# Kernel optimization log

Hardware: AMD Instinct MI355X
Metric: run time of the kernel (lower is better)

## Reference

```python
import jax, jax.numpy as jnp
import numpy as np

N = 200000          # occupied pillars
H = W = 512         # pseudo_image_dims
C = 32              # feat_channels == embed_dim
HEADS = 2
DH = C // HEADS     # 16
SHIFTS = np.array([[0, 0], [-1, 0], [1, 0], [0, 1], [-1, 1], [1, 1], [0, -1], [-1, -1], [1, -1]], dtype=np.int32)  # INDEX_SHIFT, 9 neighbors


def setup_inputs() -> dict:
    key = jax.random.key(0)
    ks = jax.random.split(key, 7)
    # unique BEV cells so the coord->index lookup is well defined
    perm = jax.random.permutation(ks[0], H * W)[:N]
    bev_coors = jnp.stack([perm // W, perm % W], axis=1).astype(jnp.int32)  # [N,2] (row, col)
    return {
        "voxel_feats": jax.random.normal(ks[1], (N, C), dtype=jnp.float32),
        "bev_coors": bev_coors,
        "pos_embedding": jax.random.normal(ks[2], (9, C), dtype=jnp.float32) * 0.02,
        "w_qkv": jax.random.normal(ks[3], (3 * C, C), dtype=jnp.float32) * 0.05,
        "b_qkv": jax.random.normal(ks[4], (3 * C,), dtype=jnp.float32) * 0.01,
        "w_out": jax.random.normal(ks[5], (C, C), dtype=jnp.float32) * 0.05,
        "b_out": jax.random.normal(ks[6], (C,), dtype=jnp.float32) * 0.01,
    }


def reference(voxel_feats, bev_coors, pos_embedding, w_qkv, b_qkv, w_out, b_out):
    shifts = jnp.asarray(SHIFTS)
    # dense lookup grid: (row, col) -> voxel index, -1 if empty
    grid = jnp.full((H, W), -1, dtype=jnp.int32)
    grid = grid.at[bev_coors[:, 0], bev_coors[:, 1]].set(jnp.arange(N, dtype=jnp.int32))

    # 9-neighbor gather with out-of-grid / empty-cell masking
    shifted = bev_coors[:, None, :] + shifts[None, :, :]                     # [N,9,2]
    in_bounds = ((shifted[..., 0] >= 0) & (shifted[..., 0] < H) &
                 (shifted[..., 1] >= 0) & (shifted[..., 1] < W))             # [N,9]
    sc = jnp.clip(shifted, 0, jnp.array([H - 1, W - 1], dtype=jnp.int32))
    nbr_idx = grid[sc[..., 0], sc[..., 1]]                                    # [N,9]
    nbr_idx = jnp.where(in_bounds, nbr_idx, -1)
    # gather neighbor feats, add per-shift positional embedding, zero invalid (masked_fill)
    kv = voxel_feats[jnp.clip(nbr_idx, 0, N - 1)] + pos_embedding[None, :, :]  # [N,9,C]
    kv = jnp.where((nbr_idx >= 0)[..., None], kv, 0.0)

    # multi-head attention: query = own feat (len 1), key/value = 9 neighbors
    wq, wk, wv = w_qkv[:C], w_qkv[C:2 * C], w_qkv[2 * C:]
    bq, bk, bv = b_qkv[:C], b_qkv[C:2 * C], b_qkv[2 * C:]
    q = (voxel_feats @ wq.T + bq).reshape(N, HEADS, DH)                      # [N,h,d]
    k = (kv @ wk.T + bk).reshape(N, 9, HEADS, DH)                            # [N,9,h,d]
    v = (kv @ wv.T + bv).reshape(N, 9, HEADS, DH)
    scores = jnp.einsum('nhd,nkhd->nhk', q, k) / jnp.sqrt(jnp.float32(DH))   # [N,h,9]
    attn = jax.nn.softmax(scores, axis=-1)
    out = jnp.einsum('nhk,nkhd->nhd', attn, v).reshape(N, C)
    out = out @ w_out.T + b_out                                              # [N,C]

    # concat and scatter to BEV pseudo-image [1, 2C, H, W]
    feat = jnp.concatenate([voxel_feats, out], axis=1)                       # [N,2C]
    canvas = jnp.zeros((2 * C, H, W), dtype=feat.dtype)
    canvas = canvas.at[:, bev_coors[:, 0], bev_coors[:, 1]].set(feat.T)
    return canvas[None]
```

## Files before the change

kernel.cpp:

```cpp
#include <hip/hip_runtime.h>
#include <hip/hip_bf16.h>

#define H_ 512
#define W_ 512
#define C_ 32
#define NPOS_ (H_ * W_)
#define TX_ 32
#define TY_ 8
#define HXX_ 34
#define HYY_ 10
#define NCELL_ (HXX_ * HYY_)
#define FST_ 40

#define CW_M 0
#define CW_U 2048
#define CW_P 2112
#define CW_R 4160

typedef float v2f __attribute__((ext_vector_type(2)));
typedef float f32x4_t __attribute__((ext_vector_type(4)));
typedef short bf16x8 __attribute__((ext_vector_type(8)));

static __device__ __forceinline__ v2f pk_add(v2f a, v2f b) {
    v2f d; asm("v_pk_add_f32 %0, %1, %2" : "=v"(d) : "v"(a), "v"(b)); return d;
}
static __device__ __forceinline__ v2f pk_fma(v2f a, v2f b, v2f c) {
    v2f d; asm("v_pk_fma_f32 %0, %1, %2, %3" : "=v"(d) : "v"(a), "v"(b), "v"(c)); return d;
}
static __device__ __forceinline__ unsigned cvt_pk_bf16(float lo, float hi) {
    unsigned r; asm("v_cvt_pk_bf16_f32 %0, %1, %2" : "=v"(r) : "v"(lo), "v"(hi)); return r;
}
static __device__ __forceinline__ short f2bf(float v) {
    __hip_bfloat16 h = __float2bfloat16(v);
    return *reinterpret_cast<short*>(&h);
}
static __device__ __forceinline__ int q_sidx(int pos, int c) {
    return pos * 64 + ((((c >> 3) ^ (pos & 7))) << 3) + (c & 7);
}
#define WFENCE() do { asm volatile("s_waitcnt lgkmcnt(0)" ::: "memory"); \
                      __builtin_amdgcn_sched_barrier(0); } while (0)

__global__ __launch_bounds__(256) void build_grid_k(const int* __restrict__ coors,
                                                    int* __restrict__ grid, int n) {
    int i = blockIdx.x * 256 + threadIdx.x;
    if (i < n) {
        int y = coors[2 * i + 0];
        int x = coors[2 * i + 1];
        grid[y * W_ + x] = i;
    }
}

__global__ __launch_bounds__(256) void prep_k(int4* __restrict__ grid4,
                                              const float* __restrict__ wqkv,
                                              const float* __restrict__ bqkv,
                                              const float* __restrict__ wout,
                                              const float* __restrict__ bout,
                                              float* __restrict__ cw) {
    if (blockIdx.x < 256) {
        grid4[blockIdx.x * 256 + threadIdx.x] = int4{-1, -1, -1, -1};
        return;
    }
    const int e0 = (int)(blockIdx.x - 256) * 256 + threadIdx.x;
    if (e0 < 2048) {
        const int i = e0 >> 6, c = e0 & 63;
        const int h = c >> 5, j = c & 31;
        float s = 0.f;
        for (int d = 0; d < 16; ++d)
            s += wqkv[(h * 16 + d) * 32 + i] * wqkv[(32 + h * 16 + d) * 32 + j];
        cw[CW_M + e0] = s;
    } else if (e0 < 4096) {
        const int e = e0 - 2048;
        const int srow = e >> 5, c = e & 31;
        const int h = srow >> 5, j = srow & 31;
        float s = 0.f;
        for (int d = 0; d < 16; ++d)
            s += wout[c * 32 + h * 16 + d] * wqkv[(64 + h * 16 + d) * 32 + j];
        cw[CW_P + e] = s;
    } else if (e0 < 4160) {
        const int e = e0 - 4096;
        const int h = e >> 5, j = e & 31;
        float s = 0.f;
        for (int d = 0; d < 16; ++d)
            s += bqkv[h * 16 + d] * wqkv[(32 + h * 16 + d) * 32 + j];
        cw[CW_U + e] = s;
    } else if (e0 < 4192) {
        const int c = e0 - 4160;
        float s = bout[c];
        for (int dv = 0; dv < 32; ++dv)
            s += wout[c * 32 + dv] * bqkv[64 + dv];
        cw[CW_R + c] = s;
    }
}

__global__ __launch_bounds__(256, 2) void fused_k(const float* __restrict__ feats,
                                                  const int* __restrict__ grid,
                                                  const float* __restrict__ pe,
                                                  const float* __restrict__ cw,
                                                  float* __restrict__ canvas) {
    __shared__ __align__(16) short flds[NCELL_ * FST_];
    __shared__ __align__(16) short qlds[256 * 64];
    __shared__ int vlds[NCELL_];
    __shared__ float pelds[288];

    const int tid = threadIdx.x;
    const int bid = blockIdx.x;
    const int tx0 = (bid & 15) * TX_;
    const int ty0 = (bid >> 4) * TY_;
    const int l15 = tid & 15;
    const int g4 = (tid >> 4) & 3;
    const int wv = tid >> 6;

    bf16x8 Bm[4];
#pragma unroll
    for (int ct = 0; ct < 4; ++ct) {
        bf16x8 b;
#pragma unroll
        for (int e = 0; e < 8; ++e)
            b[e] = f2bf(cw[CW_M + (8 * g4 + e) * 64 + ct * 16 + l15]);
        Bm[ct] = b;
    }
    bf16x8 Bp[2][2];
#pragma unroll
    for (int kc = 0; kc < 2; ++kc)
#pragma unroll
        for (int ct = 0; ct < 2; ++ct) {
            bf16x8 b;
#pragma unroll
            for (int e = 0; e < 8; ++e)
                b[e] = f2bf(cw[CW_P + (kc * 32 + 8 * g4 + e) * 32 + ct * 16 + l15]);
            Bp[kc][ct] = b;
        }
    float uq[4];
#pragma unroll
    for (int ct = 0; ct < 4; ++ct) uq[ct] = cw[CW_U + ct * 16 + l15];
    float rch[2];
#pragma unroll
    for (int ct = 0; ct < 2; ++ct) rch[ct] = cw[CW_R + ct * 16 + l15];

    for (int c = tid; c < 288; c += 256) pelds[c] = pe[c];
    for (int c = tid; c < NCELL_; c += 256) {
        const int hy = c / HXX_, hx = c - hy * HXX_;
        const int gy = ty0 + hy - 1, gx = tx0 + hx - 1;
        int vi = -1;
        if (((unsigned)gy < (unsigned)H_) && ((unsigned)gx < (unsigned)W_))
            vi = grid[gy * W_ + gx];
        vlds[c] = vi;
        uint4 wq[4];
        if (vi >= 0) {
            const float* src = feats + (size_t)vi * 32;
#pragma unroll
            for (int q = 0; q < 4; ++q) {
                const float4 va = *reinterpret_cast<const float4*>(src + q * 8);
                const float4 vb = *reinterpret_cast<const float4*>(src + q * 8 + 4);
                wq[q].x = cvt_pk_bf16(va.x, va.y);
                wq[q].y = cvt_pk_bf16(va.z, va.w);
                wq[q].z = cvt_pk_bf16(vb.x, vb.y);
                wq[q].w = cvt_pk_bf16(vb.z, vb.w);
            }
        } else {
            wq[0] = wq[1] = wq[2] = wq[3] = uint4{0u, 0u, 0u, 0u};
        }
#pragma unroll
        for (int q = 0; q < 4; ++q)
            *reinterpret_cast<uint4*>(flds + c * FST_ + q * 8) = wq[q];
    }
    __syncthreads();

    f32x4_t accq[4][4];
#pragma unroll
    for (int i = 0; i < 4; ++i) {
        const int rt = wv * 4 + i;
        const int pr = rt * 16 + l15;
        const int oc = ((pr >> 5) + 1) * HXX_ + (pr & 31) + 1;
        const bf16x8 af = *reinterpret_cast<const bf16x8*>(flds + oc * FST_ + 8 * g4);
#pragma unroll
        for (int ct = 0; ct < 4; ++ct) {
            f32x4_t acc = {uq[ct], uq[ct], uq[ct], uq[ct]};
            accq[i][ct] = __builtin_amdgcn_mfma_f32_16x16x32_bf16(af, Bm[ct], acc, 0, 0, 0);
        }
    }
#pragma unroll
    for (int i = 0; i < 4; ++i) {
        const int p0 = (wv * 4 + i) * 16 + g4 * 4;
#pragma unroll
        for (int ct = 0; ct < 4; ++ct) {
            const int c = ct * 16 + l15;
            const unsigned w01 = cvt_pk_bf16(accq[i][ct][0], accq[i][ct][1]);
            const unsigned w23 = cvt_pk_bf16(accq[i][ct][2], accq[i][ct][3]);
            qlds[q_sidx(p0 + 0, c)] = (short)(w01 & 0xffffu);
            qlds[q_sidx(p0 + 1, c)] = (short)(w01 >> 16);
            qlds[q_sidx(p0 + 2, c)] = (short)(w23 & 0xffffu);
            qlds[q_sidx(p0 + 3, c)] = (short)(w23 >> 16);
        }
    }
    WFENCE();

    const int lx = tid & 31, ly = tid >> 5;
    const int p = (ty0 + ly) * W_ + tx0 + lx;
    const int pos = tid;
    const int ocell = (ly + 1) * HXX_ + lx + 1;
    const bool occ = vlds[ocell] >= 0;

    {
        const short* fb = flds + ocell * FST_;
#pragma unroll
        for (int q = 0; q < 4; ++q) {
            const uint4 w = *reinterpret_cast<const uint4*>(fb + q * 8);
            const unsigned uu[4] = {w.x, w.y, w.z, w.w};
#pragma unroll
            for (int d = 0; d < 4; ++d) {
                const int j = q * 8 + d * 2;
                canvas[(size_t)j * NPOS_ + p] = __uint_as_float(uu[d] << 16);
                canvas[(size_t)(j + 1) * NPOS_ + p] = __uint_as_float(uu[d] & 0xffff0000u);
            }
        }
    }

    if (occ) {
        v2f qk0[16], qk1[16];
#pragma unroll
        for (int cb = 0; cb < 8; ++cb) {
            const uint4 w = *reinterpret_cast<const uint4*>(qlds + pos * 64 + ((cb ^ (pos & 7)) << 3));
            const unsigned uu[4] = {w.x, w.y, w.z, w.w};
#pragma unroll
            for (int d = 0; d < 4; ++d) {
                const int jj = cb * 4 + d;
                v2f qv;
                qv.x = __uint_as_float(uu[d] << 16);
                qv.y = __uint_as_float(uu[d] & 0xffff0000u);
                if (jj < 16) qk0[jj] = qv; else qk1[jj - 16] = qv;
            }
        }
        float l0 = 0.f, l1 = 0.f;
        v2f g0[16], g1[16];
#pragma unroll
        for (int j = 0; j < 16; ++j) { g0[j] = v2f{0.f, 0.f}; g1[j] = v2f{0.f, 0.f}; }

        const int DYv[9] = {0, -1, 1, 0, -1, 1, 0, -1, 1};
        const int DXv[9] = {0, 0, 0, 1, 1, 1, -1, -1, -1};
#pragma unroll
        for (int k = 0; k < 9; ++k) {
            const int cell = (ly + 1 + DYv[k]) * HXX_ + (lx + 1 + DXv[k]);
            const bool val = vlds[cell] >= 0;
            const short* fb = flds + cell * FST_;
            v2f t[16];
#pragma unroll
            for (int q = 0; q < 4; ++q) {
                const uint4 w = *reinterpret_cast<const uint4*>(fb + q * 8);
                const unsigned uu[4] = {w.x, w.y, w.z, w.w};
#pragma unroll
                for (int d = 0; d < 4; ++d) {
                    const int jj = q * 4 + d;
                    v2f tv;
                    tv.x = __uint_as_float(uu[d] << 16);
                    tv.y = __uint_as_float(uu[d] & 0xffff0000u);
                    t[jj] = pk_add(tv, *reinterpret_cast<const v2f*>(pelds + k * 32 + 2 * jj));
                }
            }
            v2f sp0{0.f, 0.f}, sp1{0.f, 0.f};
#pragma unroll
            for (int j = 0; j < 16; ++j) {
                sp0 = pk_fma(qk0[j], t[j], sp0);
                sp1 = pk_fma(qk1[j], t[j], sp1);
            }
            const float e0 = __expf((sp0.x + sp0.y) * 0.25f);
            const float e1 = __expf((sp1.x + sp1.y) * 0.25f);
            l0 += val ? e0 : 1.f;
            l1 += val ? e1 : 1.f;
            const float w0 = val ? e0 : 0.f;
            const float w1 = val ? e1 : 0.f;
            const v2f w0v{w0, w0}, w1v{w1, w1};
#pragma unroll
            for (int j = 0; j < 16; ++j) {
                g0[j] = pk_fma(w0v, t[j], g0[j]);
                g1[j] = pk_fma(w1v, t[j], g1[j]);
            }
        }
        const float inv0 = 1.f / l0, inv1 = 1.f / l1;
#pragma unroll
        for (int cb = 0; cb < 8; ++cb) {
            unsigned wd[4];
#pragma unroll
            for (int d = 0; d < 4; ++d) {
                const int jj = cb * 4 + d;
                const v2f gg = (jj < 16) ? g0[jj] : g1[jj - 16];
                const float iv = (jj < 16) ? inv0 : inv1;
                wd[d] = cvt_pk_bf16(gg.x * iv, gg.y * iv);
            }
            const uint4 w{wd[0], wd[1], wd[2], wd[3]};
            *reinterpret_cast<uint4*>(qlds + pos * 64 + ((cb ^ (pos & 7)) << 3)) = w;
        }
    } else {
        const uint4 z{0u, 0u, 0u, 0u};
#pragma unroll
        for (int cb = 0; cb < 8; ++cb)
            *reinterpret_cast<uint4*>(qlds + pos * 64 + ((cb ^ (pos & 7)) << 3)) = z;
    }
    WFENCE();

    f32x4_t acco[4][2];
#pragma unroll
    for (int i = 0; i < 4; ++i) {
        const int pr = (wv * 4 + i) * 16 + l15;
        const bf16x8 a0 = *reinterpret_cast<const bf16x8*>(qlds + pr * 64 + (((0 + g4) ^ (pr & 7)) << 3));
        const bf16x8 a1 = *reinterpret_cast<const bf16x8*>(qlds + pr * 64 + (((4 + g4) ^ (pr & 7)) << 3));
#pragma unroll
        for (int ct = 0; ct < 2; ++ct) {
            f32x4_t acc = {0.f, 0.f, 0.f, 0.f};
            acc = __builtin_amdgcn_mfma_f32_16x16x32_bf16(a0, Bp[0][ct], acc, 0, 0, 0);
            acc = __builtin_amdgcn_mfma_f32_16x16x32_bf16(a1, Bp[1][ct], acc, 0, 0, 0);
            acco[i][ct] = acc;
        }
    }
#pragma unroll
    for (int i = 0; i < 4; ++i) {
        const int pt0 = (wv * 4 + i) * 16 + g4 * 4;
        const int yy = pt0 >> 5, xx = pt0 & 31;
        bool ok[4];
#pragma unroll
        for (int r = 0; r < 4; ++r) {
            const int pt = pt0 + r;
            ok[r] = vlds[((pt >> 5) + 1) * HXX_ + (pt & 31) + 1] >= 0;
        }
#pragma unroll
        for (int ct = 0; ct < 2; ++ct) {
            const int ch = 32 + ct * 16 + l15;
            float4 ov;
            ov.x = ok[0] ? acco[i][ct][0] + rch[ct] : 0.f;
            ov.y = ok[1] ? acco[i][ct][1] + rch[ct] : 0.f;
            ov.z = ok[2] ? acco[i][ct][2] + rch[ct] : 0.f;
            ov.w = ok[3] ? acco[i][ct][3] + rch[ct] : 0.f;
            *reinterpret_cast<float4*>(&canvas[(size_t)ch * NPOS_ + (ty0 + yy) * W_ + tx0 + xx]) = ov;
        }
    }
}

extern "C" void kernel_launch(void* const* d_in, const int* in_sizes, int n_in,
                              void* d_out, int out_size, void* d_ws, size_t ws_size,
                              hipStream_t stream) {
    const float* feats = (const float*)d_in[0];
    const int*   coors = (const int*)d_in[1];
    const float* pe    = (const float*)d_in[2];
    const float* wqkv  = (const float*)d_in[3];
    const float* bqkv  = (const float*)d_in[4];
    const float* wout  = (const float*)d_in[5];
    const float* bout  = (const float*)d_in[6];
    float* canvas = (float*)d_out;

    const int n = in_sizes[0] / C_;
    int* grid = (int*)d_ws;
    float* cw = (float*)((char*)d_ws + NPOS_ * sizeof(int));

    prep_k<<<273, 256, 0, stream>>>((int4*)grid, wqkv, bqkv, wout, bout, cw);
    build_grid_k<<<(n + 255) / 256, 256, 0, stream>>>(coors, grid, n);
    fused_k<<<(W_ / TX_) * (H_ / TY_), 256, 0, stream>>>(feats, grid, pe, cw, canvas);
}
```

Baseline: 46.80 us.

## Split attention into two passes with per-head threads to halve LDS and registers

Restructures the fused kernel so each wave handles its 64 positions in two batches of 32. The query projection, the attention and the output projection run per batch. Within a batch each thread computes one head for one position instead of both heads, which halves per-thread register arrays. The q buffer in LDS shrinks to 128 rows, and launch bounds are raised to 3 blocks per CU to gain occupancy. In exchange there are more wave fences and loop iterations, each neighbor feature is loaded and unpacked twice (once per head), and the extra occupancy may force register spills.

After: 74.97 us. 60.2% more time.

```diff
diff --git a/kernel.cpp b/kernel.cpp
--- a/kernel.cpp
+++ b/kernel.cpp
@@ -34,8 +34,8 @@
     __hip_bfloat16 h = __float2bfloat16(v);
     return *reinterpret_cast<short*>(&h);
 }
-static __device__ __forceinline__ int q_sidx(int pos, int c) {
-    return pos * 64 + ((((c >> 3) ^ (pos & 7))) << 3) + (c & 7);
+static __device__ __forceinline__ int q_sidx(int row, int c) {
+    return row * 64 + ((((c >> 3) ^ (row & 7))) << 3) + (c & 7);
 }
 #define WFENCE() do { asm volatile("s_waitcnt lgkmcnt(0)" ::: "memory"); \
                       __builtin_amdgcn_sched_barrier(0); } while (0)
@@ -92,13 +92,13 @@
     }
 }
 
-__global__ __launch_bounds__(256, 2) void fused_k(const float* __restrict__ feats,
+__global__ __launch_bounds__(256, 3) void fused_k(const float* __restrict__ feats,
                                                   const int* __restrict__ grid,
                                                   const float* __restrict__ pe,
                                                   const float* __restrict__ cw,
                                                   float* __restrict__ canvas) {
     __shared__ __align__(16) short flds[NCELL_ * FST_];
-    __shared__ __align__(16) short qlds[256 * 64];
+    __shared__ __align__(16) short qlds[128 * 64];
     __shared__ int vlds[NCELL_];
     __shared__ float pelds[288];
 
@@ -166,43 +166,10 @@
     }
     __syncthreads();
 
-    f32x4_t accq[4][4];
-#pragma unroll
-    for (int i = 0; i < 4; ++i) {
-        const int rt = wv * 4 + i;
-        const int pr = rt * 16 + l15;
-        const int oc = ((pr >> 5) + 1) * HXX_ + (pr & 31) + 1;
-        const bf16x8 af = *reinterpret_cast<const bf16x8*>(flds + oc * FST_ + 8 * g4);
-#pragma unroll
-        for (int ct = 0; ct < 4; ++ct) {
-            f32x4_t acc = {uq[ct], uq[ct], uq[ct], uq[ct]};
-            accq[i][ct] = __builtin_amdgcn_mfma_f32_16x16x32_bf16(af, Bm[ct], acc, 0, 0, 0);
-        }
-    }
-#pragma unroll
-    for (int i = 0; i < 4; ++i) {
-        const int p0 = (wv * 4 + i) * 16 + g4 * 4;
-#pragma unroll
-        for (int ct = 0; ct < 4; ++ct) {
-            const int c = ct * 16 + l15;
-            const unsigned w01 = cvt_pk_bf16(accq[i][ct][0], accq[i][ct][1]);
-            const unsigned w23 = cvt_pk_bf16(accq[i][ct][2], accq[i][ct][3]);
-            qlds[q_sidx(p0 + 0, c)] = (short)(w01 & 0xffffu);
-            qlds[q_sidx(p0 + 1, c)] = (short)(w01 >> 16);
-            qlds[q_sidx(p0 + 2, c)] = (short)(w23 & 0xffffu);
-            qlds[q_sidx(p0 + 3, c)] = (short)(w23 >> 16);
-        }
-    }
-    WFENCE();
-
-    const int lx = tid & 31, ly = tid >> 5;
-    const int p = (ty0 + ly) * W_ + tx0 + lx;
-    const int pos = tid;
-    const int ocell = (ly + 1) * HXX_ + lx + 1;
-    const bool occ = vlds[ocell] >= 0;
-
     {
-        const short* fb = flds + ocell * FST_;
+        const int lx = tid & 31, ly = tid >> 5;
+        const int p = (ty0 + ly) * W_ + tx0 + lx;
+        const short* fb = flds + ((ly + 1) * HXX_ + lx + 1) * FST_;
 #pragma unroll
         for (int q = 0; q < 4; ++q) {
             const uint4 w = *reinterpret_cast<const uint4*>(fb + q * 8);
@@ -216,122 +183,151 @@
         }
     }
 
-    if (occ) {
-        v2f qk0[16], qk1[16];
-#pragma unroll
-        for (int cb = 0; cb < 8; ++cb) {
-            const uint4 w = *reinterpret_cast<const uint4*>(qlds + pos * 64 + ((cb ^ (pos & 7)) << 3));
-            const unsigned uu[4] = {w.x, w.y, w.z, w.w};
-#pragma unroll
-            for (int d = 0; d < 4; ++d) {
-                const int jj = cb * 4 + d;
-                v2f qv;
-                qv.x = __uint_as_float(uu[d] << 16);
-                qv.y = __uint_as_float(uu[d] & 0xffff0000u);
-                if (jj < 16) qk0[jj] = qv; else qk1[jj - 16] = qv;
-            }
-        }
-        float l0 = 0.f, l1 = 0.f;
-        v2f g0[16], g1[16];
-#pragma unroll
-        for (int j = 0; j < 16; ++j) { g0[j] = v2f{0.f, 0.f}; g1[j] = v2f{0.f, 0.f}; }
-
-        const int DYv[9] = {0, -1, 1, 0, -1, 1, 0, -1, 1};
-        const int DXv[9] = {0, 0, 0, 1, 1, 1, -1, -1, -1};
-#pragma unroll
-        for (int k = 0; k < 9; ++k) {
-            const int cell = (ly + 1 + DYv[k]) * HXX_ + (lx + 1 + DXv[k]);
-            const bool val = vlds[cell] >= 0;
-            const short* fb = flds + cell * FST_;
-            v2f t[16];
-#pragma unroll
-            for (int q = 0; q < 4; ++q) {
-                const uint4 w = *reinterpret_cast<const uint4*>(fb + q * 8);
-                const unsigned uu[4] = {w.x, w.y, w.z, w.w};
-#pragma unroll
-                for (int d = 0; d < 4; ++d) {
-                    const int jj = q * 4 + d;
-                    v2f tv;
-                    tv.x = __uint_as_float(uu[d] << 16);
-                    tv.y = __uint_as_float(uu[d] & 0xffff0000u);
-                    t[jj] = pk_add(tv, *reinterpret_cast<const v2f*>(pelds + k * 32 + 2 * jj));
+    const int DYv[9] = {0, -1, 1, 0, -1, 1, 0, -1, 1};
+    const int DXv[9] = {0, 0, 0, 1, 1, 1, -1, -1, -1};
+    const int hh = (tid >> 5) & 1;
+    const int m31 = tid & 31;
+    const int qrow0 = wv * 32;
+
+    for (int b = 0; b < 2; ++b) {
+#pragma unroll
+        for (int ii = 0; ii < 2; ++ii) {
+            const int pr = (wv * 4 + b * 2 + ii) * 16 + l15;
+            const int oc = ((pr >> 5) + 1) * HXX_ + (pr & 31) + 1;
+            const bf16x8 af = *reinterpret_cast<const bf16x8*>(flds + oc * FST_ + 8 * g4);
+            f32x4_t accq[4];
+#pragma unroll
+            for (int ct = 0; ct < 4; ++ct) {
+                f32x4_t acc = {uq[ct], uq[ct], uq[ct], uq[ct]};
+                accq[ct] = __builtin_amdgcn_mfma_f32_16x16x32_bf16(af, Bm[ct], acc, 0, 0, 0);
+            }
+            const int r0 = qrow0 + ii * 16 + g4 * 4;
+#pragma unroll
+            for (int ct = 0; ct < 4; ++ct) {
+                const int c = ct * 16 + l15;
+                const unsigned w01 = cvt_pk_bf16(accq[ct][0], accq[ct][1]);
+                const unsigned w23 = cvt_pk_bf16(accq[ct][2], accq[ct][3]);
+                qlds[q_sidx(r0 + 0, c)] = (short)(w01 & 0xffffu);
+                qlds[q_sidx(r0 + 1, c)] = (short)(w01 >> 16);
+                qlds[q_sidx(r0 + 2, c)] = (short)(w23 & 0xffffu);
+                qlds[q_sidx(r0 + 3, c)] = (short)(w23 >> 16);
+            }
+        }
+        WFENCE();
+
+        {
+            const int pos = wv * 64 + b * 32 + m31;
+            const int ply = pos >> 5, plx = pos & 31;
+            const int socell = (ply + 1) * HXX_ + plx + 1;
+            const int srow = qrow0 + m31;
+            if (vlds[socell] >= 0) {
+                v2f qk[16];
+#pragma unroll
+                for (int cc = 0; cc < 4; ++cc) {
+                    const uint4 w = *reinterpret_cast<const uint4*>(
+                        qlds + srow * 64 + (((4 * hh + cc) ^ (srow & 7)) << 3));
+                    const unsigned uu[4] = {w.x, w.y, w.z, w.w};
+#pragma unroll
+                    for (int d = 0; d < 4; ++d) {
+                        v2f qv;
+                        qv.x = __uint_as_float(uu[d] << 16);
+                        qv.y = __uint_as_float(uu[d] & 0xffff0000u);
+                        qk[cc * 4 + d] = qv;
+                    }
                 }
-            }
-            v2f sp0{0.f, 0.f}, sp1{0.f, 0.f};
-#pragma unroll
-            for (int j = 0; j < 16; ++j) {
-                sp0 = pk_fma(qk0[j], t[j], sp0);
-                sp1 = pk_fma(qk1[j], t[j], sp1);
-            }
-            const float e0 = __expf((sp0.x + sp0.y) * 0.25f);
-            const float e1 = __expf((sp1.x + sp1.y) * 0.25f);
-            l0 += val ? e0 : 1.f;
-            l1 += val ? e1 : 1.f;
-            const float w0 = val ? e0 : 0.f;
-            const float w1 = val ? e1 : 0.f;
-            const v2f w0v{w0, w0}, w1v{w1, w1};
-#pragma unroll
-            for (int j = 0; j < 16; ++j) {
-                g0[j] = pk_fma(w0v, t[j], g0[j]);
-                g1[j] = pk_fma(w1v, t[j], g1[j]);
-            }
-        }
-        const float inv0 = 1.f / l0, inv1 = 1.f / l1;
-#pragma unroll
-        for (int cb = 0; cb < 8; ++cb) {
-            unsigned wd[4];
-#pragma unroll
-            for (int d = 0; d < 4; ++d) {
-                const int jj = cb * 4 + d;
-                const v2f gg = (jj < 16) ? g0[jj] : g1[jj - 16];
-                const float iv = (jj < 16) ? inv0 : inv1;
-                wd[d] = cvt_pk_bf16(gg.x * iv, gg.y * iv);
-            }
-            const uint4 w{wd[0], wd[1], wd[2], wd[3]};
-            *reinterpret_cast<uint4*>(qlds + pos * 64 + ((cb ^ (pos & 7)) << 3)) = w;
-        }
-    } else {
-        const uint4 z{0u, 0u, 0u, 0u};
-#pragma unroll
-        for (int cb = 0; cb < 8; ++cb)
-            *reinterpret_cast<uint4*>(qlds + pos * 64 + ((cb ^ (pos & 7)) << 3)) = z;
-    }
-    WFENCE();
-
-    f32x4_t acco[4][2];
-#pragma unroll
-    for (int i = 0; i < 4; ++i) {
-        const int pr = (wv * 4 + i) * 16 + l15;
-        const bf16x8 a0 = *reinterpret_cast<const bf16x8*>(qlds + pr * 64 + (((0 + g4) ^ (pr & 7)) << 3));
-        const bf16x8 a1 = *reinterpret_cast<const bf16x8*>(qlds + pr * 64 + (((4 + g4) ^ (pr & 7)) << 3));
-#pragma unroll
-        for (int ct = 0; ct < 2; ++ct) {
-            f32x4_t acc = {0.f, 0.f, 0.f, 0.f};
-            acc = __builtin_amdgcn_mfma_f32_16x16x32_bf16(a0, Bp[0][ct], acc, 0, 0, 0);
-            acc = __builtin_amdgcn_mfma_f32_16x16x32_bf16(a1, Bp[1][ct], acc, 0, 0, 0);
-            acco[i][ct] = acc;
-        }
-    }
-#pragma unroll
-    for (int i = 0; i < 4; ++i) {
-        const int pt0 = (wv * 4 + i) * 16 + g4 * 4;
-        const int yy = pt0 >> 5, xx = pt0 & 31;
-        bool ok[4];
-#pragma unroll
-        for (int r = 0; r < 4; ++r) {
-            const int pt = pt0 + r;
-            ok[r] = vlds[((pt >> 5) + 1) * HXX_ + (pt & 31) + 1] >= 0;
-        }
-#pragma unroll
-        for (int ct = 0; ct < 2; ++ct) {
-            const int ch = 32 + ct * 16 + l15;
-            float4 ov;
-            ov.x = ok[0] ? acco[i][ct][0] + rch[ct] : 0.f;
-            ov.y = ok[1] ? acco[i][ct][1] + rch[ct] : 0.f;
-            ov.z = ok[2] ? acco[i][ct][2] + rch[ct] : 0.f;
-            ov.w = ok[3] ? acco[i][ct][3] + rch[ct] : 0.f;
-            *reinterpret_cast<float4*>(&canvas[(size_t)ch * NPOS_ + (ty0 + yy) * W_ + tx0 + xx]) = ov;
-        }
+                float l = 0.f;
+                v2f g[16];
+#pragma unroll
+                for (int m = 0; m < 16; ++m) g[m] = v2f{0.f, 0.f};
+
+#pragma unroll
+                for (int k = 0; k < 9; ++k) {
+                    const int cell = (ply + 1 + DYv[k]) * HXX_ + (plx + 1 + DXv[k]);
+                    const bool val = vlds[cell] >= 0;
+                    const short* fb = flds + cell * FST_;
+                    v2f t[16];
+#pragma unroll
+                    for (int q = 0; q < 4; ++q) {
+                        const uint4 w = *reinterpret_cast<const uint4*>(fb + q * 8);
+                        const unsigned uu[4] = {w.x, w.y, w.z, w.w};
+#pragma unroll
+                        for (int d = 0; d < 4; ++d) {
+                            const int jj = q * 4 + d;
+                            v2f tv;
+                            tv.x = __uint_as_float(uu[d] << 16);
+                            tv.y = __uint_as_float(uu[d] & 0xffff0000u);
+                            t[jj] = pk_add(tv, *reinterpret_cast<const v2f*>(
+                                pelds + k * 32 + 2 * jj));
+                        }
+                    }
+                    v2f sp{0.f, 0.f};
+#pragma unroll
+                    for (int m = 0; m < 16; ++m) sp = pk_fma(qk[m], t[m], sp);
+                    const float s = sp.x + sp.y;
+                    const float e = __expf(s * 0.25f);
+                    l += val ? e : 1.f;
+                    const float wgt = val ? e : 0.f;
+                    const v2f wv2{wgt, wgt};
+#pragma unroll
+                    for (int m = 0; m < 16; ++m) g[m] = pk_fma(wv2, t[m], g[m]);
+                }
+                const float inv = 1.f / l;
+#pragma unroll
+                for (int cc = 0; cc < 4; ++cc) {
+                    unsigned wd[4];
+#pragma unroll
+                    for (int d = 0; d < 4; ++d)
+                        wd[d] = cvt_pk_bf16(g[cc * 4 + d].x * inv, g[cc * 4 + d].y * inv);
+                    const uint4 w{wd[0], wd[1], wd[2], wd[3]};
+                    *reinterpret_cast<uint4*>(
+                        qlds + srow * 64 + (((4 * hh + cc) ^ (srow & 7)) << 3)) = w;
+                }
+            } else {
+                const uint4 z{0u, 0u, 0u, 0u};
+#pragma unroll
+                for (int cc = 0; cc < 4; ++cc)
+                    *reinterpret_cast<uint4*>(
+                        qlds + srow * 64 + (((4 * hh + cc) ^ (srow & 7)) << 3)) = z;
+            }
+        }
+        WFENCE();
+
+#pragma unroll
+        for (int ii = 0; ii < 2; ++ii) {
+            const int gr = qrow0 + ii * 16 + l15;
+            const bf16x8 a0 = *reinterpret_cast<const bf16x8*>(
+                qlds + gr * 64 + (((0 + g4) ^ (gr & 7)) << 3));
+            const bf16x8 a1 = *reinterpret_cast<const bf16x8*>(
+                qlds + gr * 64 + (((4 + g4) ^ (gr & 7)) << 3));
+            f32x4_t acco[2];
+#pragma unroll
+            for (int ct = 0; ct < 2; ++ct) {
+                f32x4_t acc = {0.f, 0.f, 0.f, 0.f};
+                acc = __builtin_amdgcn_mfma_f32_16x16x32_bf16(a0, Bp[0][ct], acc, 0, 0, 0);
+                acc = __builtin_amdgcn_mfma_f32_16x16x32_bf16(a1, Bp[1][ct], acc, 0, 0, 0);
+                acco[ct] = acc;
+            }
+            const int pt0 = (wv * 4 + b * 2 + ii) * 16 + g4 * 4;
+            const int yy = pt0 >> 5, xx = pt0 & 31;
+            bool ok[4];
+#pragma unroll
+            for (int r = 0; r < 4; ++r) {
+                const int pt = pt0 + r;
+                ok[r] = vlds[((pt >> 5) + 1) * HXX_ + (pt & 31) + 1] >= 0;
+            }
+#pragma unroll
+            for (int ct = 0; ct < 2; ++ct) {
+                const int ch = 32 + ct * 16 + l15;
+                float4 ov;
+                ov.x = ok[0] ? acco[ct][0] + rch[ct] : 0.f;
+                ov.y = ok[1] ? acco[ct][1] + rch[ct] : 0.f;
+                ov.z = ok[2] ? acco[ct][2] + rch[ct] : 0.f;
+                ov.w = ok[3] ? acco[ct][3] + rch[ct] : 0.f;
+                *reinterpret_cast<float4*>(
+                    &canvas[(size_t)ch * NPOS_ + (ty0 + yy) * W_ + tx0 + xx]) = ov;
+            }
+        }
+        WFENCE();
     }
 }
 
```
